# Kernel tuning notes

Measured on AMD Instinct MI355X. Metric: run time of the kernel, lower is better.

Reference implementation:

```python
import jax, jax.numpy as jnp
import numpy as np

N_NODES = 25000
N_EDGES = 400000
IN_DIM, HID_DIM, OUT_DIM = 174, 128, 64


def setup_inputs() -> dict:
    key = jax.random.key(0)
    ks = jax.random.split(key, 8)
    x = jax.random.normal(ks[0], (N_NODES, IN_DIM), dtype=jnp.float32)
    edge_index = jax.random.randint(ks[1], (2, N_EDGES), 0, N_NODES, dtype=jnp.int64)
    # PyG SAGEConv params: lin_l (neighbors, with bias), lin_r (root, no bias)
    def glorot(k, shape):
        lim = float(np.sqrt(6.0 / (shape[0] + shape[1])))
        return jax.random.uniform(k, shape, jnp.float32, -lim, lim)
    W1_l = glorot(ks[2], (HID_DIM, IN_DIM))
    W1_r = glorot(ks[3], (HID_DIM, IN_DIM))
    b1 = jnp.zeros((HID_DIM,), jnp.float32)
    W2_l = glorot(ks[4], (OUT_DIM, HID_DIM))
    W2_r = glorot(ks[5], (OUT_DIM, HID_DIM))
    b2 = jnp.zeros((OUT_DIM,), jnp.float32)
    return {"x": x, "edge_index": edge_index, "W1_l": W1_l, "b1": b1,
            "W1_r": W1_r, "W2_l": W2_l, "b2": b2, "W2_r": W2_r}


def _sage_conv(h, src, dst, W_l, b, W_r):
    # mean-aggregate neighbor features at destination nodes
    msg = h[src]                                       # [E, F] gather
    summed = jax.ops.segment_sum(msg, dst, num_segments=N_NODES)  # [N, F]
    deg = jax.ops.segment_sum(jnp.ones((src.shape[0],), h.dtype), dst,
                              num_segments=N_NODES)    # [N]
    mean = summed / jnp.maximum(deg, 1.0)[:, None]
    # out = lin_l(mean) + lin_r(h)
    return mean @ W_l.T + b + h @ W_r.T


def reference(x, edge_index, W1_l, b1, W1_r, W2_l, b2, W2_r):
    src, dst = edge_index[0], edge_index[1]
    h = _sage_conv(x, src, dst, W1_l, b1, W1_r)
    h = jax.nn.relu(h)
    # dropout is identity in eval mode (module exposes freeze() for inference)
    out = _sage_conv(h, src, dst, W2_l, b2, W2_r)
    return out
```

## Files before the change

### kernel.cpp

```cpp
#include <hip/hip_runtime.h>

#define N_NODES 25000
#define N_EDGES 400000
#define IN_DIM 174
#define HID_DIM 128
#define OUT_DIM 64
#define MPAD 25088
#define BINCAP 64

using u32 = unsigned int;
typedef __attribute__((ext_vector_type(8))) short s16x8;
typedef __attribute__((ext_vector_type(4))) float f32x4;
typedef __attribute__((ext_vector_type(4))) u32 u32x4;

__device__ __forceinline__ float bflo(u32 u) { u32 t = u << 16; return __builtin_bit_cast(float, t); }
__device__ __forceinline__ float bfhi(u32 u) { u32 t = u & 0xffff0000u; return __builtin_bit_cast(float, t); }
__device__ __forceinline__ u32 f2b(float f) {
    u32 u = __builtin_bit_cast(u32, f);
    return (u + 0x7fffu + ((u >> 16) & 1u)) >> 16;
}
__device__ __forceinline__ u32 packbf2(float a, float b) { return f2b(a) | (f2b(b) << 16); }

__device__ __forceinline__ void gload_lds16(const void* g, void* l) {
    __builtin_amdgcn_global_load_lds(
        (const __attribute__((address_space(1))) u32*)g,
        (__attribute__((address_space(3))) u32*)l, 16, 0, 0);
}

#define XB4_CNT (N_NODES * 24)
#define WB1_CNT (256 * 96)
#define WB2_CNT (128 * 64)
#define PREP_TOT (XB4_CNT + WB1_CNT + WB2_CNT + N_NODES)

__global__ __launch_bounds__(256) void prep_all_kernel(
    const float* __restrict__ x,
    const float* __restrict__ W1l, const float* __restrict__ W1r,
    const float* __restrict__ W2l, const float* __restrict__ W2r,
    u32* __restrict__ xb, u32* __restrict__ wb1, u32* __restrict__ wb2,
    int* __restrict__ degI) {
    int idx = blockIdx.x * blockDim.x + threadIdx.x;
    if (idx < XB4_CNT) {
        int n = idx / 24, d8 = idx - n * 24;
        const float* xr = x + (size_t)n * IN_DIM;
        u32x4 o;
        #pragma unroll
        for (int q = 0; q < 4; ++q) {
            int d2 = d8 * 4 + q;
            float2 v = make_float2(0.f, 0.f);
            if (d2 < 87) v = ((const float2*)xr)[d2];
            o[q] = packbf2(v.x, v.y);
        }
        *(u32x4*)(xb + (size_t)n * 96 + d8 * 4) = o;
        return;
    }
    idx -= XB4_CNT;
    if (idx < WB1_CNT) {
        int nrow = idx / 96, d2 = idx - nrow * 96;
        const float* src = (nrow < 128) ? W1l + (size_t)nrow * IN_DIM
                                        : W1r + (size_t)(nrow - 128) * IN_DIM;
        float2 v = make_float2(0.f, 0.f);
        if (d2 < 87) v = ((const float2*)src)[d2];
        wb1[idx] = packbf2(v.x, v.y);
        return;
    }
    idx -= WB1_CNT;
    if (idx < WB2_CNT) {
        int nrow = idx >> 6, d2 = idx & 63;
        const float* src = (nrow < 64) ? W2l + (size_t)nrow * HID_DIM
                                       : W2r + (size_t)(nrow - 64) * HID_DIM;
        float2 v = ((const float2*)src)[d2];
        wb2[idx] = packbf2(v.x, v.y);
        return;
    }
    idx -= WB2_CNT;
    if (idx < N_NODES) degI[idx] = 0;
}

__global__ void fill_bin_kernel(const int* __restrict__ ei, int* __restrict__ degI,
                                int* __restrict__ bins) {
    int e2 = (blockIdx.x * blockDim.x + threadIdx.x) * 2;
    if (e2 < N_EDGES) {
        int2 s = *(const int2*)(ei + e2);
        int2 t = *(const int2*)(ei + N_EDGES + e2);
        int p0 = atomicAdd(&degI[t.x], 1);
        if (p0 < BINCAP) bins[t.x * BINCAP + p0] = s.x;
        int p1 = atomicAdd(&degI[t.y], 1);
        if (p1 < BINCAP) bins[t.y * BINCAP + p1] = s.y;
    }
}

template <int K, int NSPLIT, int BM>
__global__ __launch_bounds__(256) void gemm_mfma(const ushort* __restrict__ A,
                                                 const ushort* __restrict__ B,
                                                 ushort* __restrict__ Cn,
                                                 ushort* __restrict__ Cr) {
    constexpr int MI = BM / 32;
    __shared__ ushort As[BM * 32];
    __shared__ ushort Bs[128 * 32];
    const int tid = threadIdx.x;
    const int lane = tid & 63, w = tid >> 6;
    const int m0 = blockIdx.x * BM;
    const int n0 = blockIdx.y * 128;
    const int wmo = (w >> 1) * (MI * 16);
    const int wno = (w & 1) * 64;

    f32x4 acc[MI][4] = {};

    const int arow = lane >> 2;
    const int achunk = (lane & 3) * 8;

    for (int kk = 0; kk < K; kk += 32) {
        #pragma unroll
        for (int c = 0; c < BM / 64; ++c) {
            int r = w * (BM / 4) + c * 16;
            gload_lds16(A + (size_t)(m0 + r + arow) * K + kk + achunk, &As[r * 32]);
        }
        #pragma unroll
        for (int c = 0; c < 2; ++c) {
            int r = w * 32 + c * 16;
            gload_lds16(B + (size_t)(n0 + r + arow) * K + kk + achunk, &Bs[r * 32]);
        }
        __syncthreads();
        s16x8 af[MI], bf[4];
        const int fr = lane & 15, fo = (lane >> 4) * 8;
        #pragma unroll
        for (int i = 0; i < MI; ++i)
            af[i] = *(const s16x8*)&As[(wmo + i * 16 + fr) * 32 + fo];
        #pragma unroll
        for (int j = 0; j < 4; ++j)
            bf[j] = *(const s16x8*)&Bs[(wno + j * 16 + fr) * 32 + fo];
        #pragma unroll
        for (int i = 0; i < MI; ++i)
            #pragma unroll
            for (int j = 0; j < 4; ++j)
                acc[i][j] = __builtin_amdgcn_mfma_f32_16x16x32_bf16(af[i], bf[j], acc[i][j], 0, 0, 0);
        __syncthreads();
    }

    const int cr = (lane >> 4) * 4, cc = lane & 15;
    #pragma unroll
    for (int i = 0; i < MI; ++i)
        #pragma unroll
        for (int r = 0; r < 4; ++r) {
            int row = m0 + wmo + i * 16 + cr + r;
            #pragma unroll
            for (int j = 0; j < 4; ++j) {
                int colg = n0 + wno + j * 16 + cc;
                ushort* Cp = (colg < NSPLIT) ? Cn : Cr;
                int c = (colg < NSPLIT) ? colg : colg - NSPLIT;
                Cp[(size_t)row * NSPLIT + c] = (ushort)f2b(acc[i][j][r]);
            }
        }
}

__global__ __launch_bounds__(256) void agg1_kernel(const u32* __restrict__ y1n,
                                                   const u32* __restrict__ y1r,
                                                   const int* __restrict__ degI,
                                                   const int* __restrict__ bins,
                                                   const float* __restrict__ b1,
                                                   u32* __restrict__ h1) {
    int w = threadIdx.x >> 6, lane = threadIdx.x & 63;
    int n = blockIdx.x * 4 + w;
    if (n >= N_NODES) return;
    int deg = degI[n];
    int d = min(deg, BINCAP);
    const int* bp = bins + n * BINCAP;
    float a0 = 0.f, a1 = 0.f;
    int j = 0;
    for (; j + 8 <= d; j += 8) {
        int4 sa = *(const int4*)(bp + j);
        int4 sb = *(const int4*)(bp + j + 4);
        u32 u0 = y1n[(size_t)sa.x * 64 + lane];
        u32 u1 = y1n[(size_t)sa.y * 64 + lane];
        u32 u2 = y1n[(size_t)sa.z * 64 + lane];
        u32 u3 = y1n[(size_t)sa.w * 64 + lane];
        u32 u4 = y1n[(size_t)sb.x * 64 + lane];
        u32 u5 = y1n[(size_t)sb.y * 64 + lane];
        u32 u6 = y1n[(size_t)sb.z * 64 + lane];
        u32 u7 = y1n[(size_t)sb.w * 64 + lane];
        a0 += bflo(u0) + bflo(u1) + bflo(u2) + bflo(u3)
            + bflo(u4) + bflo(u5) + bflo(u6) + bflo(u7);
        a1 += bfhi(u0) + bfhi(u1) + bfhi(u2) + bfhi(u3)
            + bfhi(u4) + bfhi(u5) + bfhi(u6) + bfhi(u7);
    }
    if (j + 4 <= d) {
        int4 s4 = *(const int4*)(bp + j);
        u32 u0 = y1n[(size_t)s4.x * 64 + lane];
        u32 u1 = y1n[(size_t)s4.y * 64 + lane];
        u32 u2 = y1n[(size_t)s4.z * 64 + lane];
        u32 u3 = y1n[(size_t)s4.w * 64 + lane];
        a0 += bflo(u0) + bflo(u1) + bflo(u2) + bflo(u3);
        a1 += bfhi(u0) + bfhi(u1) + bfhi(u2) + bfhi(u3);
        j += 4;
    }
    for (; j < d; ++j) {
        int s = bp[j];
        u32 u = y1n[(size_t)s * 64 + lane];
        a0 += bflo(u); a1 += bfhi(u);
    }
    float inv = 1.f / fmaxf((float)deg, 1.f);
    u32 ur = y1r[(size_t)n * 64 + lane];
    float2 bb = ((const float2*)b1)[lane];
    float v0 = fmaxf(a0 * inv + bflo(ur) + bb.x, 0.f);
    float v1 = fmaxf(a1 * inv + bfhi(ur) + bb.y, 0.f);
    h1[(size_t)n * 64 + lane] = packbf2(v0, v1);
}

__global__ __launch_bounds__(256) void agg2_kernel(const u32* __restrict__ y2n,
                                                   const u32* __restrict__ y2r,
                                                   const int* __restrict__ degI,
                                                   const int* __restrict__ bins,
                                                   const float* __restrict__ b2,
                                                   float2* __restrict__ out) {
    int w = threadIdx.x >> 6, lane = threadIdx.x & 63;
    int half = lane >> 5, dd = lane & 31;
    int n = blockIdx.x * 4 + w;
    if (n >= N_NODES) return;
    int deg = degI[n];
    int d = min(deg, BINCAP);
    const int* bp = bins + n * BINCAP;
    float a0 = 0.f, a1 = 0.f;
    int j = 0;
    for (; j + 8 <= d; j += 8) {
        int s0 = bp[j + half],     s1 = bp[j + 2 + half];
        int s2 = bp[j + 4 + half], s3 = bp[j + 6 + half];
        u32 u0 = y2n[(size_t)s0 * 32 + dd];
        u32 u1 = y2n[(size_t)s1 * 32 + dd];
        u32 u2 = y2n[(size_t)s2 * 32 + dd];
        u32 u3 = y2n[(size_t)s3 * 32 + dd];
        a0 += bflo(u0) + bflo(u1) + bflo(u2) + bflo(u3);
        a1 += bfhi(u0) + bfhi(u1) + bfhi(u2) + bfhi(u3);
    }
    if (j + 4 <= d) {
        int s0 = bp[j + half], s1 = bp[j + 2 + half];
        u32 u0 = y2n[(size_t)s0 * 32 + dd];
        u32 u1 = y2n[(size_t)s1 * 32 + dd];
        a0 += bflo(u0) + bflo(u1);
        a1 += bfhi(u0) + bfhi(u1);
        j += 4;
    }
    if (j + 2 <= d) {
        int s = bp[j + half];
        u32 u = y2n[(size_t)s * 32 + dd];
        a0 += bflo(u); a1 += bfhi(u);
        j += 2;
    }
    if (j < d && half == 0) {
        int s = bp[j];
        u32 u = y2n[(size_t)s * 32 + dd];
        a0 += bflo(u); a1 += bfhi(u);
    }
    a0 += __shfl_xor(a0, 32, 64);
    a1 += __shfl_xor(a1, 32, 64);
    if (half == 0) {
        float inv = 1.f / fmaxf((float)deg, 1.f);
        u32 ur = y2r[(size_t)n * 32 + dd];
        float2 bb = ((const float2*)b2)[dd];
        float2 o;
        o.x = a0 * inv + bflo(ur) + bb.x;
        o.y = a1 * inv + bfhi(ur) + bb.y;
        out[(size_t)n * 32 + dd] = o;
    }
}


extern "C" void kernel_launch(void* const* d_in, const int* in_sizes, int n_in,
                              void* d_out, int out_size, void* d_ws, size_t ws_size,
                              hipStream_t stream) {
    const float* x   = (const float*)d_in[0];
    const int*   ei  = (const int*)d_in[1];
    const float* W1l = (const float*)d_in[2];
    const float* b1  = (const float*)d_in[3];
    const float* W1r = (const float*)d_in[4];
    const float* W2l = (const float*)d_in[5];
    const float* b2  = (const float*)d_in[6];
    const float* W2r = (const float*)d_in[7];

    char* w = (char*)d_ws;
    auto alloc = [&](size_t bytes) -> char* {
        char* p = w;
        w += (bytes + 255) & ~(size_t)255;
        return p;
    };
    int* degI = (int*)alloc((size_t)N_NODES * 4);
    int* bins = (int*)alloc((size_t)N_NODES * BINCAP * 4);
    u32* wb1  = (u32*)alloc((size_t)WB1_CNT * 4);
    u32* wb2  = (u32*)alloc((size_t)WB2_CNT * 4);
    u32* xb   = (u32*)alloc((size_t)MPAD * 96 * 4);
    u32* y1n  = (u32*)alloc((size_t)MPAD * 64 * 4);
    u32* y1r  = (u32*)alloc((size_t)MPAD * 64 * 4);
    u32* y2n  = (u32*)alloc((size_t)MPAD * 32 * 4);
    u32* y2r  = (u32*)alloc((size_t)MPAD * 32 * 4);
    u32* h1   = xb;

    prep_all_kernel<<<(PREP_TOT + 255) / 256, 256, 0, stream>>>(
        x, W1l, W1r, W2l, W2r, xb, wb1, wb2, degI);
    fill_bin_kernel<<<(N_EDGES / 2 + 255) / 256, 256, 0, stream>>>(ei, degI, bins);

    gemm_mfma<192, 128, 128><<<dim3(196, 2), 256, 0, stream>>>(
        (const ushort*)xb, (const ushort*)wb1, (ushort*)y1n, (ushort*)y1r);
    agg1_kernel<<<(N_NODES + 3) / 4, 256, 0, stream>>>(y1n, y1r, degI, bins, b1, h1);
    gemm_mfma<128, 64, 64><<<dim3(392, 1), 256, 0, stream>>>(
        (const ushort*)h1, (const ushort*)wb2, (ushort*)y2n, (ushort*)y2r);
    agg2_kernel<<<(N_NODES + 3) / 4, 256, 0, stream>>>(y2n, y2r, degI, bins, b2, (float2*)d_out);
}
```

Measured before the change: 83.39 us.

## Fuse x bf16 conversion into layer-1 GEMM and co-schedule edge binning blocks

Drops the separate pass that converts x to a padded bf16 buffer. The first GEMM now reads fp32 x directly, converting and packing it into LDS on the fly. The edge-binning work becomes extra blocks of the same launch, so binning runs concurrently with the GEMM and one kernel launch plus one full round trip of x through memory are removed. In exchange, the A-tile load is a synchronous per-thread float2 load instead of an async global-to-LDS copy, and because each x tile is read by both N blocks, the fp32 conversion is done twice. h1 now gets its own buffer.

```diff
diff --git a/kernel.cpp b/kernel.cpp
--- a/kernel.cpp
+++ b/kernel.cpp
@@ -27,33 +27,15 @@
         (__attribute__((address_space(3))) u32*)l, 16, 0, 0);
 }
 
-#define XB4_CNT (N_NODES * 24)
 #define WB1_CNT (256 * 96)
 #define WB2_CNT (128 * 64)
-#define PREP_TOT (XB4_CNT + WB1_CNT + WB2_CNT + N_NODES)
-
-__global__ __launch_bounds__(256) void prep_all_kernel(
-    const float* __restrict__ x,
+#define PREP_TOT (WB1_CNT + WB2_CNT + N_NODES)
+
+__global__ __launch_bounds__(256) void prep_w_kernel(
     const float* __restrict__ W1l, const float* __restrict__ W1r,
     const float* __restrict__ W2l, const float* __restrict__ W2r,
-    u32* __restrict__ xb, u32* __restrict__ wb1, u32* __restrict__ wb2,
-    int* __restrict__ degI) {
+    u32* __restrict__ wb1, u32* __restrict__ wb2, int* __restrict__ degI) {
     int idx = blockIdx.x * blockDim.x + threadIdx.x;
-    if (idx < XB4_CNT) {
-        int n = idx / 24, d8 = idx - n * 24;
-        const float* xr = x + (size_t)n * IN_DIM;
-        u32x4 o;
-        #pragma unroll
-        for (int q = 0; q < 4; ++q) {
-            int d2 = d8 * 4 + q;
-            float2 v = make_float2(0.f, 0.f);
-            if (d2 < 87) v = ((const float2*)xr)[d2];
-            o[q] = packbf2(v.x, v.y);
-        }
-        *(u32x4*)(xb + (size_t)n * 96 + d8 * 4) = o;
-        return;
-    }
-    idx -= XB4_CNT;
     if (idx < WB1_CNT) {
         int nrow = idx / 96, d2 = idx - nrow * 96;
         const float* src = (nrow < 128) ? W1l + (size_t)nrow * IN_DIM
@@ -76,17 +58,100 @@
     if (idx < N_NODES) degI[idx] = 0;
 }
 
-__global__ void fill_bin_kernel(const int* __restrict__ ei, int* __restrict__ degI,
-                                int* __restrict__ bins) {
-    int e2 = (blockIdx.x * blockDim.x + threadIdx.x) * 2;
-    if (e2 < N_EDGES) {
-        int2 s = *(const int2*)(ei + e2);
-        int2 t = *(const int2*)(ei + N_EDGES + e2);
-        int p0 = atomicAdd(&degI[t.x], 1);
-        if (p0 < BINCAP) bins[t.x * BINCAP + p0] = s.x;
-        int p1 = atomicAdd(&degI[t.y], 1);
-        if (p1 < BINCAP) bins[t.y * BINCAP + p1] = s.y;
-    }
+#define G1_GEMM_BLOCKS 392
+#define G1_EDGE_BLOCKS ((N_EDGES / 4 + 255) / 256)
+
+__global__ __launch_bounds__(256) void gemm1_fused_kernel(
+    const float* __restrict__ x, const ushort* __restrict__ wb1,
+    ushort* __restrict__ y1n, ushort* __restrict__ y1r,
+    const int* __restrict__ ei, int* __restrict__ degI, int* __restrict__ bins) {
+    const int bid = blockIdx.x;
+    const int tid = threadIdx.x;
+
+    if (bid >= G1_GEMM_BLOCKS) {
+        int e4 = ((bid - G1_GEMM_BLOCKS) * 256 + tid) * 4;
+        if (e4 < N_EDGES) {
+            int4 s = *(const int4*)(ei + e4);
+            int4 t = *(const int4*)(ei + N_EDGES + e4);
+            int p0 = atomicAdd(&degI[t.x], 1);
+            if (p0 < BINCAP) bins[t.x * BINCAP + p0] = s.x;
+            int p1 = atomicAdd(&degI[t.y], 1);
+            if (p1 < BINCAP) bins[t.y * BINCAP + p1] = s.y;
+            int p2 = atomicAdd(&degI[t.z], 1);
+            if (p2 < BINCAP) bins[t.z * BINCAP + p2] = s.z;
+            int p3 = atomicAdd(&degI[t.w], 1);
+            if (p3 < BINCAP) bins[t.w * BINCAP + p3] = s.w;
+        }
+        return;
+    }
+
+    __shared__ ushort As[128 * 32];
+    __shared__ ushort Bs[128 * 32];
+    const int lane = tid & 63, w = tid >> 6;
+    const int gy = bid / 196, gx = bid - gy * 196;
+    const int m0 = gx * 128, n0 = gy * 128;
+    const int wmo = (w >> 1) * 64;
+    const int wno = (w & 1) * 64;
+
+    f32x4 acc[4][4] = {};
+
+    const int arow = lane >> 2;
+    const int achunk = (lane & 3) * 8;
+    const int r4 = tid >> 2;
+    const int q  = tid & 3;
+
+    for (int kk = 0; kk < 192; kk += 32) {
+        #pragma unroll
+        for (int c = 0; c < 2; ++c) {
+            int r = w * 32 + c * 16;
+            gload_lds16(wb1 + (size_t)(n0 + r + arow) * 192 + kk + achunk, &Bs[r * 32]);
+        }
+        #pragma unroll
+        for (int it = 0; it < 2; ++it) {
+            int r = it * 64 + r4;
+            int gm = m0 + r;
+            int c0 = kk + q * 8;
+            u32x4 o;
+            #pragma unroll
+            for (int e = 0; e < 4; ++e) {
+                int col = c0 + e * 2;
+                float2 v = make_float2(0.f, 0.f);
+                if (gm < N_NODES && col < IN_DIM)
+                    v = *(const float2*)(x + (size_t)gm * IN_DIM + col);
+                o[e] = packbf2(v.x, v.y);
+            }
+            ((u32x4*)As)[r * 4 + q] = o;
+        }
+        __syncthreads();
+        s16x8 af[4], bf[4];
+        const int fr = lane & 15, fo = (lane >> 4) * 8;
+        #pragma unroll
+        for (int i = 0; i < 4; ++i) {
+            af[i] = *(const s16x8*)&As[(wmo + i * 16 + fr) * 32 + fo];
+            bf[i] = *(const s16x8*)&Bs[(wno + i * 16 + fr) * 32 + fo];
+        }
+        #pragma unroll
+        for (int i = 0; i < 4; ++i)
+            #pragma unroll
+            for (int j = 0; j < 4; ++j)
+                acc[i][j] = __builtin_amdgcn_mfma_f32_16x16x32_bf16(af[i], bf[j], acc[i][j], 0, 0, 0);
+        __syncthreads();
+    }
+
+    const int cr = (lane >> 4) * 4, cc = lane & 15;
+    #pragma unroll
+    for (int i = 0; i < 4; ++i)
+        #pragma unroll
+        for (int r = 0; r < 4; ++r) {
+            int row = m0 + wmo + i * 16 + cr + r;
+            #pragma unroll
+            for (int j = 0; j < 4; ++j) {
+                int colg = n0 + wno + j * 16 + cc;
+                ushort* Cp = (colg < 128) ? y1n : y1r;
+                int c = colg & 127;
+                Cp[(size_t)row * 128 + c] = (ushort)f2b(acc[i][j][r]);
+            }
+        }
 }
 
 template <int K, int NSPLIT, int BM>
@@ -286,19 +351,16 @@
     int* bins = (int*)alloc((size_t)N_NODES * BINCAP * 4);
     u32* wb1  = (u32*)alloc((size_t)WB1_CNT * 4);
     u32* wb2  = (u32*)alloc((size_t)WB2_CNT * 4);
-    u32* xb   = (u32*)alloc((size_t)MPAD * 96 * 4);
     u32* y1n  = (u32*)alloc((size_t)MPAD * 64 * 4);
     u32* y1r  = (u32*)alloc((size_t)MPAD * 64 * 4);
+    u32* h1   = (u32*)alloc((size_t)MPAD * 64 * 4);
     u32* y2n  = (u32*)alloc((size_t)MPAD * 32 * 4);
     u32* y2r  = (u32*)alloc((size_t)MPAD * 32 * 4);
-    u32* h1   = xb;
-
-    prep_all_kernel<<<(PREP_TOT + 255) / 256, 256, 0, stream>>>(
-        x, W1l, W1r, W2l, W2r, xb, wb1, wb2, degI);
-    fill_bin_kernel<<<(N_EDGES / 2 + 255) / 256, 256, 0, stream>>>(ei, degI, bins);
-
-    gemm_mfma<192, 128, 128><<<dim3(196, 2), 256, 0, stream>>>(
-        (const ushort*)xb, (const ushort*)wb1, (ushort*)y1n, (ushort*)y1r);
+
+    prep_w_kernel<<<(PREP_TOT + 255) / 256, 256, 0, stream>>>(
+        W1l, W1r, W2l, W2r, wb1, wb2, degI);
+    gemm1_fused_kernel<<<G1_GEMM_BLOCKS + G1_EDGE_BLOCKS, 256, 0, stream>>>(
+        x, (const ushort*)wb1, (ushort*)y1n, (ushort*)y1r, ei, degI, bins);
     agg1_kernel<<<(N_NODES + 3) / 4, 256, 0, stream>>>(y1n, y1r, degI, bins, b1, h1);
     gemm_mfma<128, 64, 64><<<dim3(392, 1), 256, 0, stream>>>(
         (const ushort*)h1, (const ushort*)wb2, (ushort*)y2n, (ushort*)y2r);
```

New measurement: 80.93 us. -2.9%, faster.
